# Optimization experiments

Measured on AMD Instinct MI355X. Metric: run time of the kernel, lower is better.

Reference implementation:

```python
import jax, jax.numpy as jnp
import numpy as np

FM = 32          # feature_maps
OUT_BITS = 16    # output_bits
PASS_STEPS = 3
N_EDGES = 3_200_000
VAR_COUNT = 100_000
CONST_COUNT = 50_000
EPS = 1e-5       # torch LayerNorm default


def _ln(x):
    # LayerNorm over last dim, elementwise_affine=False
    mu = jnp.mean(x, axis=-1, keepdims=True)
    var = jnp.mean((x - mu) ** 2, axis=-1, keepdims=True)
    return (x - mu) / jnp.sqrt(var + EPS)


def _mlp_ln(x, W1, b1, W2, b2):
    # Linear -> ReLU -> Linear -> LayerNorm(no affine)
    return _ln(jax.nn.relu(x @ W1 + b1) @ W2 + b2)


def _linear_init(key, fan_in, fan_out):
    kW, kb = jax.random.split(key)
    bound = 1.0 / np.sqrt(fan_in)
    W = jax.random.uniform(kW, (fan_in, fan_out), jnp.float32, -bound, bound)
    b = jax.random.uniform(kb, (fan_out,), jnp.float32, -bound, bound)
    return W, b


def setup_inputs() -> dict:
    key = jax.random.key(0)
    ks = jax.random.split(key, 12)
    inp = {}
    inp["edge_var"] = jax.random.randint(ks[0], (N_EDGES,), 0, VAR_COUNT, dtype=jnp.int64 if jax.config.jax_enable_x64 else jnp.int32)
    inp["edge_const"] = jax.random.randint(ks[1], (N_EDGES,), 0, CONST_COUNT, dtype=jnp.int64 if jax.config.jax_enable_x64 else jnp.int32)
    inp["edge_val"] = jax.random.normal(ks[2], (N_EDGES,), jnp.float32)
    inp["conditions_values"] = jax.random.normal(ks[3], (CONST_COUNT,), jnp.float32)
    inp["var_count"] = VAR_COUNT
    inp["const_count"] = CONST_COUNT
    # prepare_cond: 1 -> 2*fm -> fm
    inp["pc_W1"], inp["pc_b1"] = _linear_init(ks[4], 1, 2 * FM)
    inp["pc_W2"], inp["pc_b2"] = _linear_init(ks[5], 2 * FM, FM)
    # constraint_update: 3*fm -> 2*fm -> fm
    inp["cu_W1"], inp["cu_b1"] = _linear_init(ks[6], 3 * FM, 2 * FM)
    inp["cu_W2"], inp["cu_b2"] = _linear_init(ks[7], 2 * FM, FM)
    # variable_update: 2*fm -> 2*fm -> fm
    inp["vu_W1"], inp["vu_b1"] = _linear_init(ks[8], 2 * FM, 2 * FM)
    inp["vu_W2"], inp["vu_b2"] = _linear_init(ks[9], 2 * FM, FM)
    # output: fm -> 2*fm -> output_bits
    inp["out_W1"], inp["out_b1"] = _linear_init(ks[10], FM, 2 * FM)
    inp["out_W2"], inp["out_b2"] = _linear_init(ks[11], 2 * FM, OUT_BITS)
    return inp


def reference(edge_var, edge_const, edge_val, conditions_values, var_count, const_count,
              pc_W1, pc_b1, pc_W2, pc_b2,
              cu_W1, cu_b1, cu_W2, cu_b2,
              vu_W1, vu_b1, vu_W2, vu_b2,
              out_W1, out_b1, out_W2, out_b2):
    variables = jnp.ones((var_count, FM), dtype=edge_val.dtype)
    emb = _mlp_ln(conditions_values[:, None], pc_W1, pc_b1, pc_W2, pc_b2)  # [C, fm]
    constraints = emb
    ev = edge_val[:, None]
    for _ in range(PASS_STEPS):
        # adj.T @ variables : scatter-add variable features into constraints
        v2c = jax.ops.segment_sum(variables[edge_var] * ev, edge_const, num_segments=const_count)
        constraints = _mlp_ln(jnp.concatenate([constraints, emb, v2c], axis=-1),
                              cu_W1, cu_b1, cu_W2, cu_b2)
        # adj @ constraints : scatter-add constraint features into variables
        c2v = jax.ops.segment_sum(constraints[edge_const] * ev, edge_var, num_segments=var_count)
        variables = _mlp_ln(jnp.concatenate([variables, c2v], axis=-1),
                            vu_W1, vu_b1, vu_W2, vu_b2)
    out = jax.nn.relu(variables @ out_W1 + out_b1) @ out_W2 + out_b2
    return jax.nn.sigmoid(out)
```

## Files before the change

kernel.cpp:

```cpp
#include <hip/hip_runtime.h>
#include <hip/hip_fp16.h>
#include <math.h>

#define FM 32
#define N_EDGES 3200000
#define VAR_COUNT 100000
#define CONST_COUNT 50000
#define LN_EPS 1e-5f

#define EPB 4096
#define ABLK 782
#define NBUCK 1563
#define BPT 7
#define AB2 784
#define CAPH 2560

typedef _Float16 f16;
typedef __attribute__((ext_vector_type(4))) _Float16 f16x4;
typedef __attribute__((ext_vector_type(4))) float f32x4;

static __device__ __forceinline__ float warp_sum32(float v) {
#pragma unroll
    for (int m = 16; m; m >>= 1) v += __shfl_xor(v, m);
    return v;
}

__global__ void init_vars(float* __restrict__ v, __half* __restrict__ v16, int n) {
    int i = blockIdx.x * 256 + threadIdx.x;
    if (i < n) {
        if (v) v[i] = 1.0f;
        if (v16) v16[i] = __float2half(1.0f);
    }
}


template <int DSHIFT>
__global__ __launch_bounds__(256) void bucket_sort(
    const int* __restrict__ dest_arr, const int* __restrict__ src_arr,
    const float* __restrict__ val_arr,
    int2* __restrict__ recs_tmp, int* __restrict__ lscan_T, int* __restrict__ rlen_T,
    int n) {
    __shared__ int hist[NBUCK];
    __shared__ int chunk[256];
    __shared__ int2 stage[EPB];
    const int t = threadIdx.x;
    const int base = blockIdx.x * EPB;
    const int nb = min(EPB, n - base);
    for (int i = t; i < NBUCK; i += 256) hist[i] = 0;
    __syncthreads();
    int dg[16], pk[16], vb[16];
#pragma unroll
    for (int k = 0; k < 16; ++k) {
        int j = k * 256 + t;
        dg[k] = -1;
        if (j < nb) {
            int dest = dest_arr[base + j];
            int src  = src_arr[base + j];
            vb[k] = __float_as_int(val_arr[base + j]);
            dg[k] = dest >> DSHIFT;
            pk[k] = ((dest & ((1 << DSHIFT) - 1)) << 20) | src;
            atomicAdd(&hist[dg[k]], 1);
        }
    }
    __syncthreads();
    int sum = 0;
#pragma unroll
    for (int k = 0; k < BPT; ++k) {
        int idx = t * BPT + k;
        if (idx < NBUCK) sum += hist[idx];
    }
    chunk[t] = sum;
    __syncthreads();
    for (int off = 1; off < 256; off <<= 1) {
        int v = (t >= off) ? chunk[t - off] : 0;
        __syncthreads();
        chunk[t] += v;
        __syncthreads();
    }
    int run = chunk[t] - sum;
#pragma unroll
    for (int k = 0; k < BPT; ++k) {
        int idx = t * BPT + k;
        if (idx < NBUCK) {
            int h = hist[idx];
            rlen_T[(size_t)idx * AB2 + blockIdx.x] = h;
            lscan_T[(size_t)idx * AB2 + blockIdx.x] = run;
            hist[idx] = run;
            run += h;
        }
    }
    __syncthreads();
#pragma unroll
    for (int k = 0; k < 16; ++k) {
        if (dg[k] >= 0) {
            int pos = atomicAdd(&hist[dg[k]], 1);
            stage[pos] = make_int2(pk[k], vb[k]);
        }
    }
    __syncthreads();
    for (int j = t; j < nb; j += 256) recs_tmp[(size_t)base + j] = stage[j];
}

__global__ __launch_bounds__(256) void row_sum(const int* __restrict__ rlen_T,
                                               int* __restrict__ btot) {
    __shared__ int ls[256];
    const int t = threadIdx.x;
    const int* rp = rlen_T + (size_t)blockIdx.x * AB2;
    int s = 0;
    for (int b = t; b < ABLK; b += 256) s += rp[b];
    ls[t] = s;
    __syncthreads();
    for (int off = 128; off; off >>= 1) {
        if (t < off) ls[t] += ls[t + off];
        __syncthreads();
    }
    if (t == 0) btot[blockIdx.x] = ls[0];
}

__global__ __launch_bounds__(256) void scan_btot(
    const int* __restrict__ btot, int* __restrict__ bb, int n, int total) {
    __shared__ int ls[256];
    const int t = threadIdx.x;
    int a[8];
    const int idx = t * 8;
    int tsum = 0;
#pragma unroll
    for (int u = 0; u < 8; ++u) {
        a[u] = (idx + u < n) ? btot[idx + u] : 0;
        tsum += a[u];
    }
    ls[t] = tsum;
    __syncthreads();
    for (int off = 1; off < 256; off <<= 1) {
        int v = (t >= off) ? ls[t - off] : 0;
        __syncthreads();
        ls[t] += v;
        __syncthreads();
    }
    int excl = ls[t] - tsum;
#pragma unroll
    for (int u = 0; u < 8; ++u) {
        if (idx + u < n) bb[idx + u] = excl;
        excl += a[u];
    }
    if (t == 0) bb[n] = total;
}


template <int DSHIFT, int NDEST>
__global__ __launch_bounds__(256) void collect_sort(
    const int2* __restrict__ recs_tmp, const int* __restrict__ lscan_T,
    const int* __restrict__ rlen_T, const int* __restrict__ bb,
    int2* __restrict__ recs_out, int* __restrict__ offs,
    float* __restrict__ wsum, int nrows) {
    __shared__ int2 stage[CAPH];
    __shared__ int rloff[256];
    __shared__ int hist[NDEST];
    __shared__ int sc[NDEST];
    __shared__ float wsumL[NDEST];
    __shared__ int nb_s;
    const int t = threadIdx.x;
    const int k = blockIdx.x;
    const int b0 = t * 4;
    int s0 = 0, s1 = 0, s2 = 0, s3 = 0, l0 = 0, l1 = 0, l2 = 0, l3 = 0;
    if (b0 + 0 < ABLK) { s0 = lscan_T[(size_t)k * AB2 + b0 + 0]; l0 = rlen_T[(size_t)k * AB2 + b0 + 0]; }
    if (b0 + 1 < ABLK) { s1 = lscan_T[(size_t)k * AB2 + b0 + 1]; l1 = rlen_T[(size_t)k * AB2 + b0 + 1]; }
    if (b0 + 2 < ABLK) { s2 = lscan_T[(size_t)k * AB2 + b0 + 2]; l2 = rlen_T[(size_t)k * AB2 + b0 + 2]; }
    if (b0 + 3 < ABLK) { s3 = lscan_T[(size_t)k * AB2 + b0 + 3]; l3 = rlen_T[(size_t)k * AB2 + b0 + 3]; }
    int tsum = l0 + l1 + l2 + l3;
    rloff[t] = tsum;
    __syncthreads();
    for (int off = 1; off < 256; off <<= 1) {
        int v = (t >= off) ? rloff[t - off] : 0;
        __syncthreads();
        rloff[t] += v;
        __syncthreads();
    }
    if (t == 255) nb_s = rloff[255];
    int o0 = rloff[t] - tsum;
    int o1 = o0 + l0, o2 = o1 + l1, o3 = o2 + l2;
    for (int i = t; i < NDEST; i += 256) { hist[i] = 0; wsumL[i] = 0.0f; }
    __syncthreads();
    const int nb = min(nb_s, CAPH);
    {
        const int2* rp = recs_tmp + (size_t)(b0 + 0) * EPB + s0;
        for (int j = 0; j < l0; ++j) if (o0 + j < CAPH) stage[o0 + j] = rp[j];
        rp = recs_tmp + (size_t)(b0 + 1) * EPB + s1;
        for (int j = 0; j < l1; ++j) if (o1 + j < CAPH) stage[o1 + j] = rp[j];
        rp = recs_tmp + (size_t)(b0 + 2) * EPB + s2;
        for (int j = 0; j < l2; ++j) if (o2 + j < CAPH) stage[o2 + j] = rp[j];
        rp = recs_tmp + (size_t)(b0 + 3) * EPB + s3;
        for (int j = 0; j < l3; ++j) if (o3 + j < CAPH) stage[o3 + j] = rp[j];
    }
    __syncthreads();
    for (int j = t; j < nb; j += 256) {
        int2 r = stage[j];
        atomicAdd(&hist[r.x >> 20], 1);
        if (wsum) atomicAdd(&wsumL[r.x >> 20], __int_as_float(r.y));
    }
    __syncthreads();
    if (t < NDEST) sc[t] = hist[t];
    __syncthreads();
    for (int off = 1; off < NDEST; off <<= 1) {
        int v = (t >= off && t < NDEST) ? sc[t - off] : 0;
        __syncthreads();
        if (t < NDEST) sc[t] += v;
        __syncthreads();
    }
    if (t < NDEST) {
        int excl = sc[t] - hist[t];
        int gd = (k << DSHIFT) + t;
        if (gd <= nrows) offs[gd] = bb[k] + excl;
        if (wsum && gd < nrows) wsum[gd] = wsumL[t];
        hist[t] = excl;
    }
    __syncthreads();
    const int base_out = bb[k];
    for (int j = t; j < nb; j += 256) {
        int2 r = stage[j];
        int pos = atomicAdd(&hist[r.x >> 20], 1);
        recs_out[(size_t)base_out + pos] = make_int2(r.x & 0xFFFFF, r.y);
    }
}


__global__ __launch_bounds__(256) void seg_gather16(
    const int* __restrict__ offs, const int2* __restrict__ recs,
    const __half* __restrict__ src16, __half* __restrict__ dst16, int nrows) {
    const int g = threadIdx.x >> 4, f2 = threadIdx.x & 15;
    const int row = blockIdx.x * 16 + g;
    if (row >= nrows) return;
    int j = offs[row];
    const int j1 = offs[row + 1];
    const __half2* __restrict__ s2 = (const __half2*)src16;
    float ax[8], ay[8];
#pragma unroll
    for (int u = 0; u < 8; ++u) { ax[u] = 0.0f; ay[u] = 0.0f; }
    for (; j + 16 <= j1; j += 16) {
        int2 r[16];
#pragma unroll
        for (int u = 0; u < 16; ++u) r[u] = recs[j + u];
        __half2 hh[16];
#pragma unroll
        for (int u = 0; u < 16; ++u) hh[u] = s2[(size_t)r[u].x * 16 + f2];
#pragma unroll
        for (int u = 0; u < 16; ++u) {
            float w = __int_as_float(r[u].y);
            float2 f = __half22float2(hh[u]);
            ax[u & 7] = fmaf(f.x, w, ax[u & 7]);
            ay[u & 7] = fmaf(f.y, w, ay[u & 7]);
        }
    }
    for (; j + 8 <= j1; j += 8) {
        int2 r[8];
#pragma unroll
        for (int u = 0; u < 8; ++u) r[u] = recs[j + u];
        __half2 hh[8];
#pragma unroll
        for (int u = 0; u < 8; ++u) hh[u] = s2[(size_t)r[u].x * 16 + f2];
#pragma unroll
        for (int u = 0; u < 8; ++u) {
            float w = __int_as_float(r[u].y);
            float2 f = __half22float2(hh[u]);
            ax[u] = fmaf(f.x, w, ax[u]);
            ay[u] = fmaf(f.y, w, ay[u]);
        }
    }
    for (; j < j1; ++j) {
        int2 ra = recs[j];
        __half2 ha = s2[(size_t)ra.x * 16 + f2];
        float wa = __int_as_float(ra.y);
        float2 fa = __half22float2(ha);
        ax[0] = fmaf(fa.x, wa, ax[0]);
        ay[0] = fmaf(fa.y, wa, ay[0]);
    }
    float rx = ((ax[0] + ax[1]) + (ax[2] + ax[3])) + ((ax[4] + ax[5]) + (ax[6] + ax[7]));
    float ry = ((ay[0] + ay[1]) + (ay[2] + ay[3])) + ((ay[4] + ay[5]) + (ay[6] + ay[7]));
    ((__half2*)dst16)[(size_t)row * 16 + f2] = __floats2half2_rn(rx, ry);
}


__global__ __launch_bounds__(256) void scatter_edges(
    const int* __restrict__ src_idx, const int* __restrict__ dst_idx,
    const float* __restrict__ ev, const float* __restrict__ src,
    float* __restrict__ dst, int n_edges) {
    int e = blockIdx.x * 8 + (threadIdx.x >> 5);
    int f = threadIdx.x & 31;
    if (e >= n_edges) return;
    atomicAdd(&dst[(size_t)dst_idx[e] * FM + f], src[(size_t)src_idx[e] * FM + f] * ev[e]);
}


template <int NSEG>
__global__ __launch_bounds__(256) void mlp_mfma(
    const __half* __restrict__ s0h, const __half* __restrict__ s1h,
    const __half* __restrict__ s2h, const float* __restrict__ ws,
    const float* __restrict__ W1, const float* __restrict__ b1,
    const float* __restrict__ W2, const float* __restrict__ b2,
    __half* __restrict__ dst16, int nrows) {
    constexpr int KT = NSEG * 2;
    __shared__ float hbuf[4][16][68];
    const int t = threadIdx.x;
    const int w = t >> 6;
    const int L = t & 63;
    const int c = L & 15;
    const int g = L >> 4;
    f16x4 B1[KT * 4];
#pragma unroll
    for (int kt = 0; kt < KT; ++kt) {
#pragma unroll
        for (int jt = 0; jt < 4; ++jt) {
            f16x4 bf;
#pragma unroll
            for (int i = 0; i < 4; ++i)
                bf[i] = (f16)W1[(size_t)(kt * 16 + 4 * g + i) * 64 + jt * 16 + c];
            B1[kt * 4 + jt] = bf;
        }
    }
    f16x4 B2[8];
#pragma unroll
    for (int kt = 0; kt < 4; ++kt) {
#pragma unroll
        for (int ct = 0; ct < 2; ++ct) {
            f16x4 bf;
#pragma unroll
            for (int i = 0; i < 4; ++i)
                bf[i] = (f16)W2[(size_t)(kt * 16 + 4 * g + i) * 32 + ct * 16 + c];
            B2[kt * 2 + ct] = bf;
        }
    }
    float b1v[4];
#pragma unroll
    for (int jt = 0; jt < 4; ++jt) b1v[jt] = b1[jt * 16 + c];
    const float b2v0 = b2[c], b2v1 = b2[16 + c];
    const f16* sa0 = (const f16*)s0h;
    const f16* sa1 = (const f16*)s1h;
    const f16* sa2 = (const f16*)s2h;

    const int step = gridDim.x * 4 * 16;
    for (int r0 = (blockIdx.x * 4 + w) * 16; r0 < nrows; r0 += step) {
        const int arow = r0 + c;
        f32x4 C1[4];
#pragma unroll
        for (int jt = 0; jt < 4; ++jt) {
            C1[jt][0] = 0.0f; C1[jt][1] = 0.0f; C1[jt][2] = 0.0f; C1[jt][3] = 0.0f;
        }
        f16x4 wsfrag;
        if (NSEG == 3 && ws) {
            f16 wv = (f16)ws[arow];
            wsfrag[0] = wv; wsfrag[1] = wv; wsfrag[2] = wv; wsfrag[3] = wv;
        }
#pragma unroll
        for (int kt = 0; kt < KT; ++kt) {
            f16x4 a;
            if (NSEG == 3 && kt >= 4 && ws) {
                a = wsfrag;
            } else {
                const f16* sp = (kt < 2) ? sa0 : ((kt < 4) ? sa1 : sa2);
                a = *(const f16x4*)(sp + (size_t)arow * FM + (kt & 1) * 16 + 4 * g);
            }
#pragma unroll
            for (int jt = 0; jt < 4; ++jt)
                C1[jt] = __builtin_amdgcn_mfma_f32_16x16x16f16(a, B1[kt * 4 + jt],
                                                               C1[jt], 0, 0, 0);
        }
#pragma unroll
        for (int jt = 0; jt < 4; ++jt)
#pragma unroll
            for (int j = 0; j < 4; ++j)
                hbuf[w][4 * g + j][jt * 16 + c] = fmaxf(C1[jt][j] + b1v[jt], 0.0f);
        asm volatile("s_waitcnt lgkmcnt(0)" ::: "memory");
        f16x4 A2[4];
#pragma unroll
        for (int kt = 0; kt < 4; ++kt) {
            float4 hv = *(const float4*)&hbuf[w][c][kt * 16 + 4 * g];
            f16x4 af;
            af[0] = (f16)hv.x; af[1] = (f16)hv.y; af[2] = (f16)hv.z; af[3] = (f16)hv.w;
            A2[kt] = af;
        }
        f32x4 C2[2];
        C2[0][0] = 0.0f; C2[0][1] = 0.0f; C2[0][2] = 0.0f; C2[0][3] = 0.0f;
        C2[1][0] = 0.0f; C2[1][1] = 0.0f; C2[1][2] = 0.0f; C2[1][3] = 0.0f;
#pragma unroll
        for (int kt = 0; kt < 4; ++kt) {
            C2[0] = __builtin_amdgcn_mfma_f32_16x16x16f16(A2[kt], B2[kt * 2 + 0],
                                                          C2[0], 0, 0, 0);
            C2[1] = __builtin_amdgcn_mfma_f32_16x16x16f16(A2[kt], B2[kt * 2 + 1],
                                                          C2[1], 0, 0, 0);
        }
#pragma unroll
        for (int j = 0; j < 4; ++j) {
            float y0 = C2[0][j] + b2v0;
            float y1 = C2[1][j] + b2v1;
            float s = y0 + y1;
            s += __shfl_xor(s, 1); s += __shfl_xor(s, 2);
            s += __shfl_xor(s, 4); s += __shfl_xor(s, 8);
            float mu = s * (1.0f / 32.0f);
            float d0 = y0 - mu, d1 = y1 - mu;
            float q = d0 * d0 + d1 * d1;
            q += __shfl_xor(q, 1); q += __shfl_xor(q, 2);
            q += __shfl_xor(q, 4); q += __shfl_xor(q, 8);
            float rs = rsqrtf(q * (1.0f / 32.0f) + LN_EPS);
            const size_t rbase = (size_t)(r0 + 4 * g + j) * FM;
            dst16[rbase + c]      = __float2half(d0 * rs);
            dst16[rbase + 16 + c] = __float2half(d1 * rs);
        }
    }
}


__global__ __launch_bounds__(256) void pc_mlp(
    const float* __restrict__ cond,
    const float* __restrict__ W1, const float* __restrict__ b1,
    const float* __restrict__ W2, const float* __restrict__ b2,
    float* __restrict__ dstA, float* __restrict__ dstB,
    __half* __restrict__ dstA16, __half* __restrict__ dstB16, int nrows) {
    __shared__ float sW2[64 * FM];
    __shared__ float sh[4][64];
    for (int i = threadIdx.x; i < 64 * FM; i += 256) sW2[i] = W2[i];
    int g = threadIdx.x >> 6, l = threadIdx.x & 63, l32 = l & 31, half = l >> 5;
    float w1l = W1[l], b1l = b1[l], b2l = b2[l32];
    __syncthreads();
    for (int row = blockIdx.x * 4 + g; row < nrows; row += gridDim.x * 4) {
        float cc = cond[row];
        sh[g][l] = fmaxf(fmaf(cc, w1l, b1l), 0.0f);
        float y = 0.0f;
#pragma unroll
        for (int k = 0; k < 32; k += 4) {
            float4 hv = *(const float4*)&sh[g][half * 32 + k];
            y = fmaf(hv.x, sW2[(half * 32 + k + 0) * FM + l32], y);
            y = fmaf(hv.y, sW2[(half * 32 + k + 1) * FM + l32], y);
            y = fmaf(hv.z, sW2[(half * 32 + k + 2) * FM + l32], y);
            y = fmaf(hv.w, sW2[(half * 32 + k + 3) * FM + l32], y);
        }
        y += __shfl_xor(y, 32);
        y += b2l;
        float s = warp_sum32(y);
        float mu = s * (1.0f / 32.0f);
        float d = y - mu;
        float v = warp_sum32(d * d);
        if (half == 0) {
            float o = d * rsqrtf(v * (1.0f / 32.0f) + LN_EPS);
            if (dstA)   dstA[(size_t)row * FM + l32] = o;
            if (dstB)   dstB[(size_t)row * FM + l32] = o;
            if (dstA16) dstA16[(size_t)row * FM + l32] = __float2half(o);
            if (dstB16) dstB16[(size_t)row * FM + l32] = __float2half(o);
        }
    }
}

template <int NSEG>
__global__ __launch_bounds__(256) void mlp_ln_f32(
    const float* __restrict__ s0, const float* __restrict__ s1,
    const float* __restrict__ s2,
    const float* __restrict__ W1, const float* __restrict__ b1,
    const float* __restrict__ W2, const float* __restrict__ b2,
    float* __restrict__ dst, __half* __restrict__ dst16, int nrows) {
    constexpr int IN = NSEG * FM;
    __shared__ float sW2[64 * FM];
    __shared__ float sx[4][IN];
    __shared__ float sh[4][64];
    for (int i = threadIdx.x; i < 64 * FM; i += 256) sW2[i] = W2[i];
    int g = threadIdx.x >> 6, l = threadIdx.x & 63, l32 = l & 31, half = l >> 5;
    float w1r[IN];
#pragma unroll
    for (int k = 0; k < IN; ++k) w1r[k] = W1[k * 64 + l];
    float b1l = b1[l], b2l = b2[l32];
    __syncthreads();
    for (int row = blockIdx.x * 4 + g; row < nrows; row += gridDim.x * 4) {
#pragma unroll
        for (int i = l; i < IN; i += 64) {
            const float* s = (i < 32) ? s0 : (i < 64) ? s1 : s2;
            sx[g][i] = s[(size_t)row * FM + (i & 31)];
        }
        float acc = b1l;
#pragma unroll
        for (int k = 0; k < IN; k += 4) {
            float4 xv = *(const float4*)&sx[g][k];
            acc = fmaf(xv.x, w1r[k + 0], acc);
            acc = fmaf(xv.y, w1r[k + 1], acc);
            acc = fmaf(xv.z, w1r[k + 2], acc);
            acc = fmaf(xv.w, w1r[k + 3], acc);
        }
        sh[g][l] = fmaxf(acc, 0.0f);
        float y = 0.0f;
#pragma unroll
        for (int k = 0; k < 32; k += 4) {
            float4 hv = *(const float4*)&sh[g][half * 32 + k];
            y = fmaf(hv.x, sW2[(half * 32 + k + 0) * FM + l32], y);
            y = fmaf(hv.y, sW2[(half * 32 + k + 1) * FM + l32], y);
            y = fmaf(hv.z, sW2[(half * 32 + k + 2) * FM + l32], y);
            y = fmaf(hv.w, sW2[(half * 32 + k + 3) * FM + l32], y);
        }
        y += __shfl_xor(y, 32);
        y += b2l;
        float s = warp_sum32(y);
        float mu = s * (1.0f / 32.0f);
        float d = y - mu;
        float v = warp_sum32(d * d);
        if (half == 0) {
            float o = d * rsqrtf(v * (1.0f / 32.0f) + LN_EPS);
            dst[(size_t)row * FM + l32] = o;
            if (dst16) dst16[(size_t)row * FM + l32] = __float2half(o);
        }
    }
}

__global__ __launch_bounds__(256) void out_mlp(
    const __half* __restrict__ x16,
    const float* __restrict__ W1, const float* __restrict__ b1,
    const float* __restrict__ W2, const float* __restrict__ b2,
    float* __restrict__ dst, int nrows) {
    __shared__ float sW2[64 * 16];
    __shared__ float sx[4][FM];
    __shared__ float sh[4][64];
    for (int i = threadIdx.x; i < 64 * 16; i += 256) sW2[i] = W2[i];
    int g = threadIdx.x >> 6, l = threadIdx.x & 63;
    int o = l & 15, q = l >> 4;
    float w1r[FM];
#pragma unroll
    for (int k = 0; k < FM; ++k) w1r[k] = W1[k * 64 + l];
    float b1l = b1[l];
    float b2o = b2[o];
    __syncthreads();
    for (int row = blockIdx.x * 4 + g; row < nrows; row += gridDim.x * 4) {
        if (l < FM) sx[g][l] = __half2float(x16[(size_t)row * FM + l]);
        float acc = b1l;
#pragma unroll
        for (int k = 0; k < FM; k += 4) {
            float4 xv = *(const float4*)&sx[g][k];
            acc = fmaf(xv.x, w1r[k + 0], acc);
            acc = fmaf(xv.y, w1r[k + 1], acc);
            acc = fmaf(xv.z, w1r[k + 2], acc);
            acc = fmaf(xv.w, w1r[k + 3], acc);
        }
        sh[g][l] = fmaxf(acc, 0.0f);
        float y = 0.0f;
#pragma unroll
        for (int k = 0; k < 16; k += 4) {
            int kk = q * 16 + k;
            float4 hv = *(const float4*)&sh[g][kk];
            y = fmaf(hv.x, sW2[(kk + 0) * 16 + o], y);
            y = fmaf(hv.y, sW2[(kk + 1) * 16 + o], y);
            y = fmaf(hv.z, sW2[(kk + 2) * 16 + o], y);
            y = fmaf(hv.w, sW2[(kk + 3) * 16 + o], y);
        }
        y += __shfl_xor(y, 16);
        y += __shfl_xor(y, 32);
        if (q == 0) dst[(size_t)row * 16 + o] = 1.0f / (1.0f + expf(-(y + b2o)));
    }
}


extern "C" void kernel_launch(void* const* d_in, const int* in_sizes, int n_in,
                              void* d_out, int out_size, void* d_ws, size_t ws_size,
                              hipStream_t stream) {
    const int*   edge_var   = (const int*)d_in[0];
    const int*   edge_const = (const int*)d_in[1];
    const float* edge_val   = (const float*)d_in[2];
    const float* cond       = (const float*)d_in[3];
    const float* pc_W1 = (const float*)d_in[6];
    const float* pc_b1 = (const float*)d_in[7];
    const float* pc_W2 = (const float*)d_in[8];
    const float* pc_b2 = (const float*)d_in[9];
    const float* cu_W1 = (const float*)d_in[10];
    const float* cu_b1 = (const float*)d_in[11];
    const float* cu_W2 = (const float*)d_in[12];
    const float* cu_b2 = (const float*)d_in[13];
    const float* vu_W1 = (const float*)d_in[14];
    const float* vu_b1 = (const float*)d_in[15];
    const float* vu_W2 = (const float*)d_in[16];
    const float* vu_b2 = (const float*)d_in[17];
    const float* out_W1 = (const float*)d_in[18];
    const float* out_b1 = (const float*)d_in[19];
    const float* out_W2 = (const float*)d_in[20];
    const float* out_b2 = (const float*)d_in[21];

    float* ws = (float*)d_ws;
    size_t off = 0;
    auto alloc = [&](size_t nelems) {
        float* p = ws + off;
        off += (nelems + 15) & ~(size_t)15;
        return p;
    };
    __half* vars16  = (__half*)alloc(VAR_COUNT * FM / 2);
    __half* cons16  = (__half*)alloc(CONST_COUNT * FM / 2);
    __half* emb16   = (__half*)alloc(CONST_COUNT * FM / 2);
    __half* msg16   = (__half*)alloc(VAR_COUNT * FM / 2);
    int2*   recs_t  = (int2*)alloc((size_t)N_EDGES * 2);
    int2*   recs_c  = (int2*)alloc((size_t)N_EDGES * 2);
    int2*   recs_v  = (int2*)alloc((size_t)N_EDGES * 2);
    int*    lscan_T = (int*)alloc((size_t)NBUCK * AB2);
    int*    rlen_T  = (int*)alloc((size_t)NBUCK * AB2);
    int*    btot    = (int*)alloc(NBUCK);
    int*    bb_c    = (int*)alloc(NBUCK + 1);
    int*    bb_v    = (int*)alloc(NBUCK + 1);
    int*    offs_c  = (int*)alloc(CONST_COUNT + 1);
    int*    offs_v  = (int*)alloc(VAR_COUNT + 1);
    float*  wsum_c  = alloc(CONST_COUNT);
    size_t need_bytes = off * sizeof(float);
    bool fast = ws_size >= need_bytes;

    float* emb  = (float*)recs_t;
    float* cons = emb + CONST_COUNT * FM;
    float* vars = cons + CONST_COUNT * FM;
    float* msg  = (float*)recs_c;

    if (fast) {
        bucket_sort<5><<<ABLK, 256, 0, stream>>>(edge_const, edge_var, edge_val,
                                                 recs_t, lscan_T, rlen_T, N_EDGES);
        row_sum<<<NBUCK, 256, 0, stream>>>(rlen_T, btot);
        scan_btot<<<1, 256, 0, stream>>>(btot, bb_c, NBUCK, N_EDGES);
        collect_sort<5, 32><<<NBUCK, 256, 0, stream>>>(
            recs_t, lscan_T, rlen_T, bb_c, recs_c, offs_c, wsum_c, CONST_COUNT);
        bucket_sort<6><<<ABLK, 256, 0, stream>>>(edge_var, edge_const, edge_val,
                                                 recs_t, lscan_T, rlen_T, N_EDGES);
        row_sum<<<NBUCK, 256, 0, stream>>>(rlen_T, btot);
        scan_btot<<<1, 256, 0, stream>>>(btot, bb_v, NBUCK, N_EDGES);
        collect_sort<6, 64><<<NBUCK, 256, 0, stream>>>(
            recs_t, lscan_T, rlen_T, bb_v, recs_v, offs_v, nullptr, VAR_COUNT);

        init_vars<<<(VAR_COUNT * FM + 255) / 256, 256, 0, stream>>>(
            nullptr, vars16, VAR_COUNT * FM);
        pc_mlp<<<1024, 256, 0, stream>>>(cond, pc_W1, pc_b1, pc_W2, pc_b2,
                                         nullptr, nullptr, emb16, cons16, CONST_COUNT);

        for (int pass = 0; pass < 3; ++pass) {
            if (pass == 0) {
                mlp_mfma<3><<<512, 256, 0, stream>>>(
                    cons16, emb16, nullptr, wsum_c,
                    cu_W1, cu_b1, cu_W2, cu_b2, cons16, CONST_COUNT);
            } else {
                seg_gather16<<<(CONST_COUNT + 15) / 16, 256, 0, stream>>>(
                    offs_c, recs_c, vars16, msg16, CONST_COUNT);
                mlp_mfma<3><<<512, 256, 0, stream>>>(
                    cons16, emb16, msg16, nullptr,
                    cu_W1, cu_b1, cu_W2, cu_b2, cons16, CONST_COUNT);
            }
            seg_gather16<<<(VAR_COUNT + 15) / 16, 256, 0, stream>>>(
                offs_v, recs_v, cons16, msg16, VAR_COUNT);
            mlp_mfma<2><<<512, 256, 0, stream>>>(
                vars16, msg16, nullptr, nullptr,
                vu_W1, vu_b1, vu_W2, vu_b2, vars16, VAR_COUNT);
        }
    } else {
        init_vars<<<(VAR_COUNT * FM + 255) / 256, 256, 0, stream>>>(
            vars, vars16, VAR_COUNT * FM);
        pc_mlp<<<1024, 256, 0, stream>>>(cond, pc_W1, pc_b1, pc_W2, pc_b2,
                                         emb, cons, nullptr, nullptr, CONST_COUNT);
        for (int pass = 0; pass < 3; ++pass) {
            hipMemsetAsync(msg, 0, (size_t)CONST_COUNT * FM * sizeof(float), stream);
            scatter_edges<<<N_EDGES / 8, 256, 0, stream>>>(edge_var, edge_const, edge_val,
                                                           vars, msg, N_EDGES);
            mlp_ln_f32<3><<<1024, 256, 0, stream>>>(cons, emb, msg,
                                                    cu_W1, cu_b1, cu_W2, cu_b2,
                                                    cons, nullptr, CONST_COUNT);
            hipMemsetAsync(msg, 0, (size_t)VAR_COUNT * FM * sizeof(float), stream);
            scatter_edges<<<N_EDGES / 8, 256, 0, stream>>>(edge_const, edge_var, edge_val,
                                                           cons, msg, N_EDGES);
            mlp_ln_f32<2><<<1024, 256, 0, stream>>>(vars, msg, nullptr,
                                                    vu_W1, vu_b1, vu_W2, vu_b2,
                                                    vars, vars16, VAR_COUNT);
        }
    }

    out_mlp<<<1024, 256, 0, stream>>>(vars16, out_W1, out_b1, out_W2, out_b2,
                                      (float*)d_out, VAR_COUNT);
}
```

Before: 469.8 us.

## Coarsen sort buckets and write bucket metadata row-major then transpose

The two-pass bucket sort now uses 782 coarser buckets, 64 or 128 destinations each, instead of 1563 buckets, so the collect stage has fewer, larger blocks with a bigger LDS staging buffer. Bucket_sort writes its per-block exclusive scan contiguously instead of as strided transposed stores, and a new tiled transpose kernel produces the transposed layout. Row lengths come from differences of adjacent scan rows, which removes the separate rlen array. This adds a transpose launch per sort and increases LDS use in collect_sort, which may reduce occupancy, and the destination histogram scan now spans up to 128 entries.

```diff
diff --git a/kernel.cpp b/kernel.cpp
--- a/kernel.cpp
+++ b/kernel.cpp
@@ -10,10 +10,10 @@
 
 #define EPB 4096
 #define ABLK 782
-#define NBUCK 1563
-#define BPT 7
+#define NB 782
 #define AB2 784
-#define CAPH 2560
+#define LSTRIDE 784
+#define CAP 4608
 
 typedef _Float16 f16;
 typedef __attribute__((ext_vector_type(4))) _Float16 f16x4;
@@ -38,15 +38,14 @@
 __global__ __launch_bounds__(256) void bucket_sort(
     const int* __restrict__ dest_arr, const int* __restrict__ src_arr,
     const float* __restrict__ val_arr,
-    int2* __restrict__ recs_tmp, int* __restrict__ lscan_T, int* __restrict__ rlen_T,
-    int n) {
-    __shared__ int hist[NBUCK];
+    int2* __restrict__ recs_tmp, int* __restrict__ lscan, int n) {
+    __shared__ int hist[NB];
     __shared__ int chunk[256];
     __shared__ int2 stage[EPB];
     const int t = threadIdx.x;
     const int base = blockIdx.x * EPB;
     const int nb = min(EPB, n - base);
-    for (int i = t; i < NBUCK; i += 256) hist[i] = 0;
+    for (int i = t; i < NB; i += 256) hist[i] = 0;
     __syncthreads();
     int dg[16], pk[16], vb[16];
 #pragma unroll
@@ -65,9 +64,9 @@
     __syncthreads();
     int sum = 0;
 #pragma unroll
-    for (int k = 0; k < BPT; ++k) {
-        int idx = t * BPT + k;
-        if (idx < NBUCK) sum += hist[idx];
+    for (int k = 0; k < 4; ++k) {
+        int idx = t * 4 + k;
+        if (idx < NB) sum += hist[idx];
     }
     chunk[t] = sum;
     __syncthreads();
@@ -79,15 +78,19 @@
     }
     int run = chunk[t] - sum;
 #pragma unroll
-    for (int k = 0; k < BPT; ++k) {
-        int idx = t * BPT + k;
-        if (idx < NBUCK) {
+    for (int k = 0; k < 4; ++k) {
+        int idx = t * 4 + k;
+        if (idx < NB) {
             int h = hist[idx];
-            rlen_T[(size_t)idx * AB2 + blockIdx.x] = h;
-            lscan_T[(size_t)idx * AB2 + blockIdx.x] = run;
             hist[idx] = run;
             run += h;
         }
+    }
+    __syncthreads();
+    {
+        int* lp = lscan + (size_t)blockIdx.x * LSTRIDE;
+        for (int i = t; i < NB; i += 256) lp[i] = hist[i];
+        if (t == 0) lp[NB] = nb;
     }
     __syncthreads();
 #pragma unroll
@@ -101,13 +104,33 @@
     for (int j = t; j < nb; j += 256) recs_tmp[(size_t)base + j] = stage[j];
 }
 
-__global__ __launch_bounds__(256) void row_sum(const int* __restrict__ rlen_T,
+__global__ __launch_bounds__(256) void transpose_meta(
+    const int* __restrict__ in, int* __restrict__ out) {
+    __shared__ int tile[32][33];
+    const int kx = blockIdx.x * 32;
+    const int by = blockIdx.y * 32;
+    const int tx = threadIdx.x & 31, ty4 = (threadIdx.x >> 5) * 4;
+#pragma unroll
+    for (int dy = 0; dy < 4; ++dy) {
+        int y = by + ty4 + dy, x = kx + tx;
+        tile[ty4 + dy][tx] = (y < ABLK && x <= NB) ? in[(size_t)y * LSTRIDE + x] : 0;
+    }
+    __syncthreads();
+#pragma unroll
+    for (int dy = 0; dy < 4; ++dy) {
+        int k = kx + ty4 + dy, b = by + tx;
+        if (k <= NB && b < ABLK) out[(size_t)k * AB2 + b] = tile[tx][ty4 + dy];
+    }
+}
+
+__global__ __launch_bounds__(256) void row_sum(const int* __restrict__ T,
                                                int* __restrict__ btot) {
     __shared__ int ls[256];
     const int t = threadIdx.x;
-    const int* rp = rlen_T + (size_t)blockIdx.x * AB2;
+    const int* r0 = T + (size_t)blockIdx.x * AB2;
+    const int* r1 = r0 + AB2;
     int s = 0;
-    for (int b = t; b < ABLK; b += 256) s += rp[b];
+    for (int b = t; b < ABLK; b += 256) s += r1[b] - r0[b];
     ls[t] = s;
     __syncthreads();
     for (int off = 128; off; off >>= 1) {
@@ -149,11 +172,11 @@
 
 template <int DSHIFT, int NDEST>
 __global__ __launch_bounds__(256) void collect_sort(
-    const int2* __restrict__ recs_tmp, const int* __restrict__ lscan_T,
-    const int* __restrict__ rlen_T, const int* __restrict__ bb,
+    const int2* __restrict__ recs_tmp, const int* __restrict__ T,
+    const int* __restrict__ bb,
     int2* __restrict__ recs_out, int* __restrict__ offs,
     float* __restrict__ wsum, int nrows) {
-    __shared__ int2 stage[CAPH];
+    __shared__ int2 stage[CAP];
     __shared__ int rloff[256];
     __shared__ int hist[NDEST];
     __shared__ int sc[NDEST];
@@ -161,13 +184,16 @@
     __shared__ int nb_s;
     const int t = threadIdx.x;
     const int k = blockIdx.x;
-    const int b0 = t * 4;
-    int s0 = 0, s1 = 0, s2 = 0, s3 = 0, l0 = 0, l1 = 0, l2 = 0, l3 = 0;
-    if (b0 + 0 < ABLK) { s0 = lscan_T[(size_t)k * AB2 + b0 + 0]; l0 = rlen_T[(size_t)k * AB2 + b0 + 0]; }
-    if (b0 + 1 < ABLK) { s1 = lscan_T[(size_t)k * AB2 + b0 + 1]; l1 = rlen_T[(size_t)k * AB2 + b0 + 1]; }
-    if (b0 + 2 < ABLK) { s2 = lscan_T[(size_t)k * AB2 + b0 + 2]; l2 = rlen_T[(size_t)k * AB2 + b0 + 2]; }
-    if (b0 + 3 < ABLK) { s3 = lscan_T[(size_t)k * AB2 + b0 + 3]; l3 = rlen_T[(size_t)k * AB2 + b0 + 3]; }
-    int tsum = l0 + l1 + l2 + l3;
+    const int* r0 = T + (size_t)k * AB2;
+    const int* r1 = r0 + AB2;
+    int s[4], l[4];
+#pragma unroll
+    for (int u = 0; u < 4; ++u) {
+        int b = t + 256 * u;
+        s[u] = 0; l[u] = 0;
+        if (b < ABLK) { s[u] = r0[b]; l[u] = r1[b] - s[u]; }
+    }
+    int tsum = l[0] + l[1] + l[2] + l[3];
     rloff[t] = tsum;
     __syncthreads();
     for (int off = 1; off < 256; off <<= 1) {
@@ -177,20 +203,16 @@
         __syncthreads();
     }
     if (t == 255) nb_s = rloff[255];
-    int o0 = rloff[t] - tsum;
-    int o1 = o0 + l0, o2 = o1 + l1, o3 = o2 + l2;
+    int o = rloff[t] - tsum;
     for (int i = t; i < NDEST; i += 256) { hist[i] = 0; wsumL[i] = 0.0f; }
     __syncthreads();
-    const int nb = min(nb_s, CAPH);
-    {
-        const int2* rp = recs_tmp + (size_t)(b0 + 0) * EPB + s0;
-        for (int j = 0; j < l0; ++j) if (o0 + j < CAPH) stage[o0 + j] = rp[j];
-        rp = recs_tmp + (size_t)(b0 + 1) * EPB + s1;
-        for (int j = 0; j < l1; ++j) if (o1 + j < CAPH) stage[o1 + j] = rp[j];
-        rp = recs_tmp + (size_t)(b0 + 2) * EPB + s2;
-        for (int j = 0; j < l2; ++j) if (o2 + j < CAPH) stage[o2 + j] = rp[j];
-        rp = recs_tmp + (size_t)(b0 + 3) * EPB + s3;
-        for (int j = 0; j < l3; ++j) if (o3 + j < CAPH) stage[o3 + j] = rp[j];
+    const int nb = min(nb_s, CAP);
+#pragma unroll
+    for (int u = 0; u < 4; ++u) {
+        int b = t + 256 * u;
+        const int2* rp = recs_tmp + (size_t)b * EPB + s[u];
+        for (int j = 0; j < l[u]; ++j) if (o + j < CAP) stage[o + j] = rp[j];
+        o += l[u];
     }
     __syncthreads();
     for (int j = t; j < nb; j += 256) {
@@ -590,11 +612,11 @@
     int2*   recs_t  = (int2*)alloc((size_t)N_EDGES * 2);
     int2*   recs_c  = (int2*)alloc((size_t)N_EDGES * 2);
     int2*   recs_v  = (int2*)alloc((size_t)N_EDGES * 2);
-    int*    lscan_T = (int*)alloc((size_t)NBUCK * AB2);
-    int*    rlen_T  = (int*)alloc((size_t)NBUCK * AB2);
-    int*    btot    = (int*)alloc(NBUCK);
-    int*    bb_c    = (int*)alloc(NBUCK + 1);
-    int*    bb_v    = (int*)alloc(NBUCK + 1);
+    int*    lscan   = (int*)alloc((size_t)ABLK * LSTRIDE);
+    int*    lscan_T = (int*)alloc((size_t)(NB + 1) * AB2);
+    int*    btot    = (int*)alloc(NB);
+    int*    bb_c    = (int*)alloc(NB + 1);
+    int*    bb_v    = (int*)alloc(NB + 1);
     int*    offs_c  = (int*)alloc(CONST_COUNT + 1);
     int*    offs_v  = (int*)alloc(VAR_COUNT + 1);
     float*  wsum_c  = alloc(CONST_COUNT);
@@ -606,19 +628,23 @@
     float* vars = cons + CONST_COUNT * FM;
     float* msg  = (float*)recs_c;
 
+    const dim3 tgrid((NB + 1 + 31) / 32, (ABLK + 31) / 32);
+
     if (fast) {
-        bucket_sort<5><<<ABLK, 256, 0, stream>>>(edge_const, edge_var, edge_val,
-                                                 recs_t, lscan_T, rlen_T, N_EDGES);
-        row_sum<<<NBUCK, 256, 0, stream>>>(rlen_T, btot);
-        scan_btot<<<1, 256, 0, stream>>>(btot, bb_c, NBUCK, N_EDGES);
-        collect_sort<5, 32><<<NBUCK, 256, 0, stream>>>(
-            recs_t, lscan_T, rlen_T, bb_c, recs_c, offs_c, wsum_c, CONST_COUNT);
-        bucket_sort<6><<<ABLK, 256, 0, stream>>>(edge_var, edge_const, edge_val,
-                                                 recs_t, lscan_T, rlen_T, N_EDGES);
-        row_sum<<<NBUCK, 256, 0, stream>>>(rlen_T, btot);
-        scan_btot<<<1, 256, 0, stream>>>(btot, bb_v, NBUCK, N_EDGES);
-        collect_sort<6, 64><<<NBUCK, 256, 0, stream>>>(
-            recs_t, lscan_T, rlen_T, bb_v, recs_v, offs_v, nullptr, VAR_COUNT);
+        bucket_sort<6><<<ABLK, 256, 0, stream>>>(edge_const, edge_var, edge_val,
+                                                 recs_t, lscan, N_EDGES);
+        transpose_meta<<<tgrid, 256, 0, stream>>>(lscan, lscan_T);
+        row_sum<<<NB, 256, 0, stream>>>(lscan_T, btot);
+        scan_btot<<<1, 256, 0, stream>>>(btot, bb_c, NB, N_EDGES);
+        collect_sort<6, 64><<<NB, 256, 0, stream>>>(
+            recs_t, lscan_T, bb_c, recs_c, offs_c, wsum_c, CONST_COUNT);
+        bucket_sort<7><<<ABLK, 256, 0, stream>>>(edge_var, edge_const, edge_val,
+                                                 recs_t, lscan, N_EDGES);
+        transpose_meta<<<tgrid, 256, 0, stream>>>(lscan, lscan_T);
+        row_sum<<<NB, 256, 0, stream>>>(lscan_T, btot);
+        scan_btot<<<1, 256, 0, stream>>>(btot, bb_v, NB, N_EDGES);
+        collect_sort<7, 128><<<NB, 256, 0, stream>>>(
+            recs_t, lscan_T, bb_v, recs_v, offs_v, nullptr, VAR_COUNT);
 
         init_vars<<<(VAR_COUNT * FM + 255) / 256, 256, 0, stream>>>(
             nullptr, vars16, VAR_COUNT * FM);
```

After: 446.2 us (median of 2 runs). 5.0% less time.
